# Kernel tuning notes

Hardware: AMD Instinct MI355X
Metric: run time of the kernel (lower is better)

## Reference

```python
import jax, jax.numpy as jnp
import numpy as np

B, T, DM, DH, DD, V, K = 2, 512, 1024, 4096, 4, 32000, 8
THR = 0.25
EPS = 1e-5
IGN = -100


def setup_inputs() -> dict:
    key = jax.random.key(0)
    ks = jax.random.split(key, 12)
    s = 0.02
    return {
        "H": jax.random.normal(ks[0], (B, T, DM), jnp.float32),
        "input_ids": jax.random.randint(ks[1], (B, T), 0, V),
        "attention_mask": jax.random.randint(ks[2], (B, T), 0, 2),
        "labels": jax.random.randint(ks[3], (B, T), 0, V),
        "emb": s * jax.random.normal(ks[4], (V, DM), jnp.float32),
        "depth_emb": s * jax.random.normal(ks[5], (DD, DM), jnp.float32),
        "ln_g": jnp.ones((DM,), jnp.float32),
        "ln_b": jnp.zeros((DM,), jnp.float32),
        "W1": s * jax.random.normal(ks[6], (DM, DH), jnp.float32),
        "b1": jnp.zeros((DH,), jnp.float32),
        "W2": s * jax.random.normal(ks[7], (DH, DM), jnp.float32),
        "b2": jnp.zeros((DM,), jnp.float32),
        "Wq": s * jax.random.normal(ks[8], (DM, V), jnp.float32),
        "bq": jnp.zeros((V,), jnp.float32),
        "Wb": s * jax.random.normal(ks[9], (DM, 1), jnp.float32),
        "bb": jnp.zeros((1,), jnp.float32),
    }


def _forward(H, input_ids, attention_mask, labels, emb, depth_emb, ln_g, ln_b, W1, b1, W2, b2, Wq, bq, Wb, bb):
    mask = attention_mask.astype(bool)  # (B,T)
    E = emb[input_ids]  # (B,T,DM)
    # draft state: broadcast over depth dim
    S = H[:, :, None, :] + E[:, :, None, :] + depth_emb[None, None]  # (B,T,DD,DM)
    mu = S.mean(-1, keepdims=True)
    var = ((S - mu) ** 2).mean(-1, keepdims=True)  # biased var, as torch LayerNorm
    S = (S - mu) * jax.lax.rsqrt(var + EPS) * ln_g + ln_b
    S = jax.nn.gelu(S @ W1 + b1, approximate=False) @ W2 + b2
    q = S @ Wq + bq  # (B,T,DD,V)
    beta = (S @ Wb + bb)[..., 0]  # (B,T,DD)
    q = jnp.where(mask[:, :, None, None], q, 0.0)
    beta = jnp.where(mask[:, :, None], beta, 0.0)
    # future labels for D depths (small fixed loop over DD)
    targets = jnp.full((B, T, DD), IGN, jnp.int32)
    valid = jnp.zeros((B, T, DD), bool)
    for d in range(1, DD + 1):
        v = mask[:, : T - d] & mask[:, d:]
        valid = valid.at[:, : T - d, d - 1].set(v)
        targets = targets.at[:, : T - d, d - 1].set(
            jnp.where(v, labels[:, d:].astype(jnp.int32), IGN))
    # token CE over valid positions (masked mean)
    logp = jax.nn.log_softmax(q, axis=-1)
    safe = jnp.where(valid, targets, 0)
    nll = -jnp.take_along_axis(logp, safe[..., None], axis=-1)[..., 0]
    cnt = valid.sum()
    L_q = jnp.where(cnt > 0, (nll * valid).sum() / jnp.maximum(cnt, 1).astype(q.dtype), jnp.zeros((), q.dtype))
    # BCE-with-logits on beta, averaged over valid source positions
    bce = jnp.logaddexp(0.0, beta) - beta * valid.astype(beta.dtype)
    src = valid.any(-1, keepdims=True)
    denom = jnp.maximum(src.sum(), 1).astype(beta.dtype)
    L_beta = (bce * src).sum() / denom
    return q, beta, L_q + L_beta


def reference(H, input_ids, attention_mask, labels, emb, depth_emb, ln_g, ln_b, W1, b1, W2, b2, Wq, bq, Wb, bb):
    q, beta, loss = _forward(H, input_ids, attention_mask, labels, emb, depth_emb,
                             ln_g, ln_b, W1, b1, W2, b2, Wq, bq, Wb, bb)
    # dynamic_branch_width
    sigma = jax.nn.sigmoid(beta)
    k = jnp.clip(jnp.ceil(sigma * float(K)).astype(jnp.int32), 1, K)
    k = jnp.where(sigma >= THR, k, 0)
    k = jnp.where(attention_mask.astype(bool)[:, :, None], k, 0)
    return q, beta, k, loss
```

## Files before the change

kernel.cpp:

```cpp
#include <hip/hip_runtime.h>
#include <math.h>

#define B_ 2
#define T_ 512
#define DM_ 1024
#define DH_ 4096
#define DD_ 4
#define V_ 32000
#define M_ 4096
#define BT_ 1024

typedef __attribute__((ext_vector_type(8))) unsigned short ushort8_t;
typedef __attribute__((ext_vector_type(4))) unsigned short ushort4_t;
typedef __attribute__((ext_vector_type(8))) __bf16 bf16x8;
typedef __attribute__((ext_vector_type(4))) float f32x4;

__device__ __forceinline__ unsigned short f2bf(float x) {
  union { float f; unsigned u; } v; v.f = x;
  unsigned r = v.u + 0x7fffu + ((v.u >> 16) & 1u);
  return (unsigned short)(r >> 16);
}
__device__ __forceinline__ float bf2f(unsigned short h) {
  union { unsigned u; float f; } v; v.u = ((unsigned)h) << 16; return v.f;
}

__device__ __forceinline__ float block_sum256(float v, float* sh) {
  #pragma unroll
  for (int o = 32; o >= 1; o >>= 1) v += __shfl_down(v, o);
  int lane = threadIdx.x & 63, wid = threadIdx.x >> 6;
  if (lane == 0) sh[wid] = v;
  __syncthreads();
  float t = sh[0] + sh[1] + sh[2] + sh[3];
  __syncthreads();
  return t;
}
__device__ __forceinline__ float block_max256(float v, float* sh) {
  #pragma unroll
  for (int o = 32; o >= 1; o >>= 1) v = fmaxf(v, __shfl_down(v, o));
  int lane = threadIdx.x & 63, wid = threadIdx.x >> 6;
  if (lane == 0) sh[wid] = v;
  __syncthreads();
  float t = fmaxf(fmaxf(sh[0], sh[1]), fmaxf(sh[2], sh[3]));
  __syncthreads();
  return t;
}

__global__ __launch_bounds__(256) void transpose_split_kernel(
    const float* __restrict__ in, int R, int C,
    unsigned short* __restrict__ out_hi, unsigned short* __restrict__ out_lo)
{
  __shared__ float tile[32][33];
  int c0 = blockIdx.x * 32, r0 = blockIdx.y * 32;
  int tx = threadIdx.x & 31, ty = threadIdx.x >> 5;
  #pragma unroll
  for (int i = 0; i < 4; ++i)
    tile[ty + i * 8][tx] = in[(size_t)(r0 + ty + i * 8) * C + c0 + tx];
  __syncthreads();
  #pragma unroll
  for (int i = 0; i < 4; ++i) {
    int orow = c0 + ty + i * 8;
    int ocol = r0 + tx;
    float v = tile[tx][ty + i * 8];
    unsigned short h = f2bf(v);
    out_hi[(size_t)orow * R + ocol] = h;
    if (out_lo) out_lo[(size_t)orow * R + ocol] = f2bf(v - bf2f(h));
  }
}

__global__ __launch_bounds__(256) void embed_ln_kernel(
    const float* __restrict__ H, const int* __restrict__ ids,
    const float* __restrict__ emb, const float* __restrict__ demb,
    const float* __restrict__ g, const float* __restrict__ be,
    unsigned short* __restrict__ Xhi, unsigned short* __restrict__ Xlo)
{
  __shared__ float sh[8];
  int m = blockIdx.x, tid = threadIdx.x;
  int bt = m >> 2, d = m & 3;
  int id = ids[bt];
  float4 x  = ((const float4*)(H   + (size_t)bt * DM_))[tid];
  float4 e  = ((const float4*)(emb + (size_t)id * DM_))[tid];
  float4 de = ((const float4*)(demb + (size_t)d * DM_))[tid];
  float v0 = x.x + e.x + de.x, v1 = x.y + e.y + de.y;
  float v2 = x.z + e.z + de.z, v3 = x.w + e.w + de.w;
  float mu = block_sum256((v0 + v1) + (v2 + v3), sh) * (1.0f / DM_);
  float d0 = v0 - mu, d1v = v1 - mu, d2 = v2 - mu, d3 = v3 - mu;
  float var = block_sum256((d0 * d0 + d1v * d1v) + (d2 * d2 + d3 * d3), sh) * (1.0f / DM_);
  float rs = rsqrtf(var + 1e-5f);
  float4 gg  = ((const float4*)g)[tid];
  float4 bb4 = ((const float4*)be)[tid];
  float y0 = d0 * rs * gg.x + bb4.x;
  float y1 = d1v * rs * gg.y + bb4.y;
  float y2 = d2 * rs * gg.z + bb4.z;
  float y3 = d3 * rs * gg.w + bb4.w;
  unsigned short h0 = f2bf(y0), h1 = f2bf(y1), h2 = f2bf(y2), h3 = f2bf(y3);
  ushort4_t hv = {h0, h1, h2, h3};
  ushort4_t lv = {f2bf(y0 - bf2f(h0)), f2bf(y1 - bf2f(h1)), f2bf(y2 - bf2f(h2)), f2bf(y3 - bf2f(h3))};
  size_t base = (size_t)m * DM_ + tid * 4;
  *(ushort4_t*)&Xhi[base] = hv;
  *(ushort4_t*)&Xlo[base] = lv;
}

__global__ __launch_bounds__(64) void w2b_kernel(
    const float* __restrict__ W2, const float* __restrict__ Wb,
    const float* __restrict__ b2, const float* __restrict__ bb,
    float* __restrict__ w2b)
{
  int j = blockIdx.x, lane = threadIdx.x;
  const float* rowp = (j < DH_) ? (W2 + (size_t)j * DM_) : b2;
  const float4* r4 = (const float4*)rowp;
  const float4* w4 = (const float4*)Wb;
  float s = 0.0f;
  for (int i = lane; i < DM_ / 4; i += 64) {
    float4 a = r4[i], w = w4[i];
    s += a.x * w.x + a.y * w.y + a.z * w.z + a.w * w.w;
  }
  #pragma unroll
  for (int o = 32; o >= 1; o >>= 1) s += __shfl_down(s, o);
  if (lane == 0) w2b[j] = (j < DH_) ? s : (s + bb[0]);
}

template<bool SPLIT, bool GELU>
__global__ __launch_bounds__(256) void gemm_kernel(
    const unsigned short* __restrict__ Ahi, const unsigned short* __restrict__ Alo,
    const unsigned short* __restrict__ Bhi, const unsigned short* __restrict__ Blo,
    const float* __restrict__ bias, int Ndim, int Kdim,
    float* __restrict__ Cf, unsigned short* __restrict__ Chi, unsigned short* __restrict__ Clo,
    const int* __restrict__ rowmask)
{
  constexpr int LDT = 40;
  __shared__ __align__(16) unsigned short sAhi[128 * LDT];
  __shared__ __align__(16) unsigned short sBhi[128 * LDT];
  __shared__ __align__(16) unsigned short sAlo[SPLIT ? 128 * LDT : 8];
  __shared__ __align__(16) unsigned short sBlo[SPLIT ? 128 * LDT : 8];
  const int n0 = blockIdx.x * 128, m0 = blockIdx.y * 128;
  const int tid = threadIdx.x, lane = tid & 63, wid = tid >> 6;
  const int wr = wid >> 1, wc = wid & 1;
  const int lrow = lane & 15, koff = (lane >> 4) * 8;
  const int rr = tid >> 2, cc = (tid & 3) * 8;

  f32x4 acc[4][4] = {};

  for (int k0 = 0; k0 < Kdim; k0 += 32) {
    __syncthreads();
    #pragma unroll
    for (int ch = 0; ch < 2; ++ch) {
      int r = rr + ch * 64;
      size_t ga = (size_t)(m0 + r) * Kdim + (k0 + cc);
      size_t gb = (size_t)(n0 + r) * Kdim + (k0 + cc);
      *(ushort8_t*)&sAhi[r * LDT + cc] = *(const ushort8_t*)&Ahi[ga];
      *(ushort8_t*)&sBhi[r * LDT + cc] = *(const ushort8_t*)&Bhi[gb];
      if constexpr (SPLIT) {
        *(ushort8_t*)&sAlo[r * LDT + cc] = *(const ushort8_t*)&Alo[ga];
        *(ushort8_t*)&sBlo[r * LDT + cc] = *(const ushort8_t*)&Blo[gb];
      }
    }
    __syncthreads();
    bf16x8 ah[4], bh[4], al[4], bl[4];
    #pragma unroll
    for (int i = 0; i < 4; ++i) {
      ah[i] = __builtin_bit_cast(bf16x8, *(const ushort8_t*)&sAhi[(wr * 64 + i * 16 + lrow) * LDT + koff]);
      bh[i] = __builtin_bit_cast(bf16x8, *(const ushort8_t*)&sBhi[(wc * 64 + i * 16 + lrow) * LDT + koff]);
      if constexpr (SPLIT) {
        al[i] = __builtin_bit_cast(bf16x8, *(const ushort8_t*)&sAlo[(wr * 64 + i * 16 + lrow) * LDT + koff]);
        bl[i] = __builtin_bit_cast(bf16x8, *(const ushort8_t*)&sBlo[(wc * 64 + i * 16 + lrow) * LDT + koff]);
      }
    }
    #pragma unroll
    for (int mi = 0; mi < 4; ++mi)
      #pragma unroll
      for (int ni = 0; ni < 4; ++ni) {
        acc[mi][ni] = __builtin_amdgcn_mfma_f32_16x16x32_bf16(ah[mi], bh[ni], acc[mi][ni], 0, 0, 0);
        if constexpr (SPLIT) {
          acc[mi][ni] = __builtin_amdgcn_mfma_f32_16x16x32_bf16(ah[mi], bl[ni], acc[mi][ni], 0, 0, 0);
          acc[mi][ni] = __builtin_amdgcn_mfma_f32_16x16x32_bf16(al[mi], bh[ni], acc[mi][ni], 0, 0, 0);
          acc[mi][ni] = __builtin_amdgcn_mfma_f32_16x16x32_bf16(al[mi], bl[ni], acc[mi][ni], 0, 0, 0);
        }
      }
  }

  #pragma unroll
  for (int mi = 0; mi < 4; ++mi) {
    #pragma unroll
    for (int ni = 0; ni < 4; ++ni) {
      int rbase = m0 + wr * 64 + mi * 16 + (lane >> 4) * 4;
      int col = n0 + wc * 64 + ni * 16 + (lane & 15);
      float bv = bias ? bias[col] : 0.0f;
      #pragma unroll
      for (int r2 = 0; r2 < 4; ++r2) {
        int gm = rbase + r2;
        float v = acc[mi][ni][r2] + bv;
        if constexpr (GELU) v = 0.5f * v * (1.0f + erff(v * 0.70710678118654752440f));
        if (rowmask) v *= (rowmask[gm >> 2] ? 1.0f : 0.0f);
        size_t idx = (size_t)gm * Ndim + col;
        if (Cf) Cf[idx] = v;
        if (Chi) {
          unsigned short h = f2bf(v);
          Chi[idx] = h;
          if (Clo) Clo[idx] = f2bf(v - bf2f(h));
        }
      }
    }
  }
}

__global__ __launch_bounds__(256) void beta_k_kernel(
    const float* __restrict__ act, const float* __restrict__ w2b,
    const int* __restrict__ mask,
    float* __restrict__ beta_out, float* __restrict__ k_out,
    float* __restrict__ bce, int* __restrict__ validf)
{
  __shared__ float sh[8];
  int m = blockIdx.x, tid = threadIdx.x;
  const float4* a4 = (const float4*)(act + (size_t)m * DH_);
  const float4* w4 = (const float4*)w2b;
  float s = 0.0f;
  for (int i = tid; i < DH_ / 4; i += 256) {
    float4 a = a4[i], w = w4[i];
    s += a.x * w.x + a.y * w.y + a.z * w.z + a.w * w.w;
  }
  float tot = block_sum256(s, sh);
  if (tid == 0) {
    int bt = m >> 2, d1 = (m & 3) + 1;
    float beta = tot + w2b[DH_];
    int mv = mask[bt];
    float bm = mv ? beta : 0.0f;
    int t = bt % T_;
    int valid = (t + d1 < T_) && mv && mask[bt + d1];
    beta_out[m] = bm;
    float sp = fmaxf(bm, 0.0f) + log1pf(expf(-fabsf(bm)));
    bce[m] = sp - (valid ? bm : 0.0f);
    validf[m] = valid;
    float sig = 1.0f / (1.0f + expf(-bm));
    int kk = (int)ceilf(sig * 8.0f);
    kk = kk < 1 ? 1 : (kk > 8 ? 8 : kk);
    if (!(sig >= 0.25f)) kk = 0;
    if (!mv) kk = 0;
    k_out[m] = (float)kk;
  }
}

__global__ __launch_bounds__(256) void ce_kernel(
    const float* __restrict__ q, const int* __restrict__ validf,
    const int* __restrict__ labels, float* __restrict__ nll)
{
  __shared__ float sh[8];
  int m = blockIdx.x, tid = threadIdx.x;
  if (!validf[m]) { if (tid == 0) nll[m] = 0.0f; return; }
  int bt = m >> 2, d1 = (m & 3) + 1;
  const float* row = q + (size_t)m * V_;
  float mx = -3.4e38f;
  for (int c = tid; c < V_; c += 256) mx = fmaxf(mx, row[c]);
  mx = block_max256(mx, sh);
  float s = 0.0f;
  for (int c = tid; c < V_; c += 256) s += expf(row[c] - mx);
  s = block_sum256(s, sh);
  if (tid == 0) {
    int tgt = labels[bt + d1];
    nll[m] = -(row[tgt] - mx - logf(s));
  }
}

__global__ __launch_bounds__(256) void loss_kernel(
    const float* __restrict__ nll, const int* __restrict__ validf,
    const float* __restrict__ bce, float* __restrict__ loss_out)
{
  __shared__ float sh[8];
  int tid = threadIdx.x;
  float snll = 0.0f, fcnt = 0.0f, sbce = 0.0f, fnsrc = 0.0f;
  for (int m = tid; m < M_; m += 256) { snll += nll[m]; fcnt += (float)validf[m]; }
  for (int bt = tid; bt < BT_; bt += 256) {
    int base = bt * 4;
    int src = validf[base] | validf[base + 1] | validf[base + 2] | validf[base + 3];
    if (src) { sbce += bce[base] + bce[base + 1] + bce[base + 2] + bce[base + 3]; fnsrc += 1.0f; }
  }
  snll = block_sum256(snll, sh);
  fcnt = block_sum256(fcnt, sh);
  sbce = block_sum256(sbce, sh);
  fnsrc = block_sum256(fnsrc, sh);
  if (tid == 0) {
    float Lq = fcnt > 0.0f ? snll / fcnt : 0.0f;
    float Lb = sbce / fmaxf(fnsrc, 1.0f);
    loss_out[0] = Lq + Lb;
  }
}

extern "C" void kernel_launch(void* const* d_in, const int* in_sizes, int n_in,
                              void* d_out, int out_size, void* d_ws, size_t ws_size,
                              hipStream_t stream) {
  const float* H    = (const float*)d_in[0];
  const int*   ids  = (const int*)d_in[1];
  const int*   mask = (const int*)d_in[2];
  const int*   labels = (const int*)d_in[3];
  const float* emb  = (const float*)d_in[4];
  const float* demb = (const float*)d_in[5];
  const float* ln_g = (const float*)d_in[6];
  const float* ln_b = (const float*)d_in[7];
  const float* W1   = (const float*)d_in[8];
  const float* b1   = (const float*)d_in[9];
  const float* W2   = (const float*)d_in[10];
  const float* b2   = (const float*)d_in[11];
  const float* Wq   = (const float*)d_in[12];
  const float* bq   = (const float*)d_in[13];
  const float* Wb   = (const float*)d_in[14];
  const float* bb   = (const float*)d_in[15];

  char* ws = (char*)d_ws; size_t off = 0;
  auto walloc = [&](size_t bytes) -> void* {
    void* p = ws + off; off = (off + bytes + 255) & ~(size_t)255; return p;
  };
  unsigned short* W1t_hi = (unsigned short*)walloc((size_t)DH_ * DM_ * 2);
  unsigned short* W1t_lo = (unsigned short*)walloc((size_t)DH_ * DM_ * 2);
  unsigned short* W2t_hi = (unsigned short*)walloc((size_t)DM_ * DH_ * 2);
  unsigned short* W2t_lo = (unsigned short*)walloc((size_t)DM_ * DH_ * 2);
  unsigned short* Wqt_hi = (unsigned short*)walloc((size_t)V_ * DM_ * 2);
  unsigned short* Xhi    = (unsigned short*)walloc((size_t)M_ * DM_ * 2);
  unsigned short* Xlo    = (unsigned short*)walloc((size_t)M_ * DM_ * 2);
  unsigned short* S2hi   = (unsigned short*)walloc((size_t)M_ * DM_ * 2);
  float* w2b   = (float*)walloc((DH_ + 1) * 4);
  float* nll   = (float*)walloc(M_ * 4);
  float* bcev  = (float*)walloc(M_ * 4);
  int*   validf = (int*)walloc(M_ * 4);

  float* q_out    = (float*)d_out;
  float* beta_out = q_out + (size_t)M_ * V_;
  float* k_out    = beta_out + M_;
  float* loss_out = k_out + M_;
  unsigned short* act_hi = (unsigned short*)d_out;
  unsigned short* act_lo = act_hi + (size_t)M_ * DH_;
  float*          act_f  = (float*)(act_lo + (size_t)M_ * DH_);

  transpose_split_kernel<<<dim3(DH_ / 32, DM_ / 32), 256, 0, stream>>>(W1, DM_, DH_, W1t_hi, W1t_lo);
  transpose_split_kernel<<<dim3(DM_ / 32, DH_ / 32), 256, 0, stream>>>(W2, DH_, DM_, W2t_hi, W2t_lo);
  transpose_split_kernel<<<dim3(V_ / 32, DM_ / 32), 256, 0, stream>>>(Wq, DM_, V_, Wqt_hi, nullptr);
  embed_ln_kernel<<<M_, 256, 0, stream>>>(H, ids, emb, demb, ln_g, ln_b, Xhi, Xlo);
  w2b_kernel<<<DH_ + 1, 64, 0, stream>>>(W2, Wb, b2, bb, w2b);
  gemm_kernel<true, true><<<dim3(DH_ / 128, M_ / 128), 256, 0, stream>>>(
      Xhi, Xlo, W1t_hi, W1t_lo, b1, DH_, DM_, act_f, act_hi, act_lo, nullptr);
  beta_k_kernel<<<M_, 256, 0, stream>>>(act_f, w2b, mask, beta_out, k_out, bcev, validf);
  gemm_kernel<true, false><<<dim3(DM_ / 128, M_ / 128), 256, 0, stream>>>(
      act_hi, act_lo, W2t_hi, W2t_lo, b2, DM_, DH_, nullptr, S2hi, nullptr, nullptr);
  gemm_kernel<false, false><<<dim3(V_ / 128, M_ / 128), 256, 0, stream>>>(
      S2hi, nullptr, Wqt_hi, nullptr, bq, V_, DM_, q_out, nullptr, nullptr, mask);
  ce_kernel<<<M_, 256, 0, stream>>>(q_out, validf, labels, nll);
  loss_kernel<<<1, 256, 0, stream>>>(nll, validf, bcev, loss_out);
}
```

Measured before the change: 1.668 ms.

## Fuse softmax and beta partials into GEMM epilogues, use direct LDS loads

The row-wise softmax max/sum and the beta dot product are computed as per-tile partials inside the GEMM epilogues, with small reduction kernels replacing full passes over q and the fp32 activation buffer. The fp32 activation write is removed. Tiles are staged with global_load_lds into unpadded LDS, the grid is swapped so row tiles vary fastest, q is written with nontemporal stores, and the lo*lo MFMA term of the split-precision product is dropped. This trades a full re-read of the large logits tensor and some precision for extra partial buffers. Unpadded LDS may cause bank conflicts.

```diff
diff --git a/kernel.cpp b/kernel.cpp
--- a/kernel.cpp
+++ b/kernel.cpp
@@ -9,6 +9,7 @@
 #define V_ 32000
 #define M_ 4096
 #define BT_ 1024
+#define NCHUNK_ 250
 
 typedef __attribute__((ext_vector_type(8))) unsigned short ushort8_t;
 typedef __attribute__((ext_vector_type(4))) unsigned short ushort4_t;
@@ -22,6 +23,22 @@
 }
 __device__ __forceinline__ float bf2f(unsigned short h) {
   union { unsigned u; float f; } v; v.u = ((unsigned)h) << 16; return v.f;
+}
+
+__device__ __forceinline__ void gload16(const void* g, void* l) {
+  __builtin_amdgcn_global_load_lds(
+      (const __attribute__((address_space(1))) void*)g,
+      (__attribute__((address_space(3))) void*)l, 16, 0, 0);
+}
+
+__device__ __forceinline__ void stage_tile(const unsigned short* src, int ld,
+                                           unsigned short* lds, int wid, int lane) {
+  #pragma unroll
+  for (int c = 0; c < 2; ++c) {
+    const int rbase = c * 64 + wid * 16;
+    const unsigned short* g = src + (size_t)(rbase + (lane >> 2)) * ld + (lane & 3) * 8;
+    gload16(g, lds + rbase * 32);
+  }
 }
 
 __device__ __forceinline__ float block_sum256(float v, float* sh) {
@@ -31,16 +48,6 @@
   if (lane == 0) sh[wid] = v;
   __syncthreads();
   float t = sh[0] + sh[1] + sh[2] + sh[3];
-  __syncthreads();
-  return t;
-}
-__device__ __forceinline__ float block_max256(float v, float* sh) {
-  #pragma unroll
-  for (int o = 32; o >= 1; o >>= 1) v = fmaxf(v, __shfl_down(v, o));
-  int lane = threadIdx.x & 63, wid = threadIdx.x >> 6;
-  if (lane == 0) sh[wid] = v;
-  __syncthreads();
-  float t = fmaxf(fmaxf(sh[0], sh[1]), fmaxf(sh[2], sh[3]));
   __syncthreads();
   return t;
 }
@@ -119,50 +126,53 @@
   if (lane == 0) w2b[j] = (j < DH_) ? s : (s + bb[0]);
 }
 
-template<bool SPLIT, bool GELU>
+template<bool SPLIT, bool GELU, bool CEPART, bool BETAPART, bool NTC>
 __global__ __launch_bounds__(256) void gemm_kernel(
     const unsigned short* __restrict__ Ahi, const unsigned short* __restrict__ Alo,
     const unsigned short* __restrict__ Bhi, const unsigned short* __restrict__ Blo,
     const float* __restrict__ bias, int Ndim, int Kdim,
     float* __restrict__ Cf, unsigned short* __restrict__ Chi, unsigned short* __restrict__ Clo,
-    const int* __restrict__ rowmask)
-{
-  constexpr int LDT = 40;
-  __shared__ __align__(16) unsigned short sAhi[128 * LDT];
-  __shared__ __align__(16) unsigned short sBhi[128 * LDT];
-  __shared__ __align__(16) unsigned short sAlo[SPLIT ? 128 * LDT : 8];
-  __shared__ __align__(16) unsigned short sBlo[SPLIT ? 128 * LDT : 8];
-  const int n0 = blockIdx.x * 128, m0 = blockIdx.y * 128;
+    const int* __restrict__ rowmask,
+    const float* __restrict__ w2bv, float* __restrict__ bpart,
+    float* __restrict__ pmax, float* __restrict__ psum)
+{
+  __shared__ __align__(16) unsigned short sAhi[128 * 32];
+  __shared__ __align__(16) unsigned short sBhi[128 * 32];
+  __shared__ __align__(16) unsigned short sAlo[SPLIT ? 128 * 32 : 8];
+  __shared__ __align__(16) unsigned short sBlo[SPLIT ? 128 * 32 : 8];
+  __shared__ float red[(CEPART || BETAPART) ? 512 : 8];
+
+  const int m0 = blockIdx.x * 128, n0 = blockIdx.y * 128;
   const int tid = threadIdx.x, lane = tid & 63, wid = tid >> 6;
   const int wr = wid >> 1, wc = wid & 1;
-  const int lrow = lane & 15, koff = (lane >> 4) * 8;
-  const int rr = tid >> 2, cc = (tid & 3) * 8;
+  const int lrow = lane & 15, koff = (lane >> 4) * 8, q4 = lane >> 4;
+
+  const unsigned short* Ab  = Ahi + (size_t)m0 * Kdim;
+  const unsigned short* Bb  = Bhi + (size_t)n0 * Kdim;
+  const unsigned short* Alb = SPLIT ? (Alo + (size_t)m0 * Kdim) : nullptr;
+  const unsigned short* Blb = SPLIT ? (Blo + (size_t)n0 * Kdim) : nullptr;
 
   f32x4 acc[4][4] = {};
 
   for (int k0 = 0; k0 < Kdim; k0 += 32) {
     __syncthreads();
-    #pragma unroll
-    for (int ch = 0; ch < 2; ++ch) {
-      int r = rr + ch * 64;
-      size_t ga = (size_t)(m0 + r) * Kdim + (k0 + cc);
-      size_t gb = (size_t)(n0 + r) * Kdim + (k0 + cc);
-      *(ushort8_t*)&sAhi[r * LDT + cc] = *(const ushort8_t*)&Ahi[ga];
-      *(ushort8_t*)&sBhi[r * LDT + cc] = *(const ushort8_t*)&Bhi[gb];
-      if constexpr (SPLIT) {
-        *(ushort8_t*)&sAlo[r * LDT + cc] = *(const ushort8_t*)&Alo[ga];
-        *(ushort8_t*)&sBlo[r * LDT + cc] = *(const ushort8_t*)&Blo[gb];
-      }
+    stage_tile(Ab + k0, Kdim, sAhi, wid, lane);
+    stage_tile(Bb + k0, Kdim, sBhi, wid, lane);
+    if constexpr (SPLIT) {
+      stage_tile(Alb + k0, Kdim, sAlo, wid, lane);
+      stage_tile(Blb + k0, Kdim, sBlo, wid, lane);
     }
+    asm volatile("s_waitcnt vmcnt(0)" ::: "memory");
     __syncthreads();
+
     bf16x8 ah[4], bh[4], al[4], bl[4];
     #pragma unroll
     for (int i = 0; i < 4; ++i) {
-      ah[i] = __builtin_bit_cast(bf16x8, *(const ushort8_t*)&sAhi[(wr * 64 + i * 16 + lrow) * LDT + koff]);
-      bh[i] = __builtin_bit_cast(bf16x8, *(const ushort8_t*)&sBhi[(wc * 64 + i * 16 + lrow) * LDT + koff]);
+      ah[i] = __builtin_bit_cast(bf16x8, *(const ushort8_t*)&sAhi[(wr * 64 + i * 16 + lrow) * 32 + koff]);
+      bh[i] = __builtin_bit_cast(bf16x8, *(const ushort8_t*)&sBhi[(wc * 64 + i * 16 + lrow) * 32 + koff]);
       if constexpr (SPLIT) {
-        al[i] = __builtin_bit_cast(bf16x8, *(const ushort8_t*)&sAlo[(wr * 64 + i * 16 + lrow) * LDT + koff]);
-        bl[i] = __builtin_bit_cast(bf16x8, *(const ushort8_t*)&sBlo[(wc * 64 + i * 16 + lrow) * LDT + koff]);
+        al[i] = __builtin_bit_cast(bf16x8, *(const ushort8_t*)&sAlo[(wr * 64 + i * 16 + lrow) * 32 + koff]);
+        bl[i] = __builtin_bit_cast(bf16x8, *(const ushort8_t*)&sBlo[(wc * 64 + i * 16 + lrow) * 32 + koff]);
       }
     }
     #pragma unroll
@@ -173,26 +183,28 @@
         if constexpr (SPLIT) {
           acc[mi][ni] = __builtin_amdgcn_mfma_f32_16x16x32_bf16(ah[mi], bl[ni], acc[mi][ni], 0, 0, 0);
           acc[mi][ni] = __builtin_amdgcn_mfma_f32_16x16x32_bf16(al[mi], bh[ni], acc[mi][ni], 0, 0, 0);
-          acc[mi][ni] = __builtin_amdgcn_mfma_f32_16x16x32_bf16(al[mi], bl[ni], acc[mi][ni], 0, 0, 0);
         }
       }
   }
 
   #pragma unroll
-  for (int mi = 0; mi < 4; ++mi) {
+  for (int mi = 0; mi < 4; ++mi)
     #pragma unroll
     for (int ni = 0; ni < 4; ++ni) {
-      int rbase = m0 + wr * 64 + mi * 16 + (lane >> 4) * 4;
-      int col = n0 + wc * 64 + ni * 16 + (lane & 15);
-      float bv = bias ? bias[col] : 0.0f;
+      const int col = n0 + wc * 64 + ni * 16 + lrow;
+      const float bv = bias ? bias[col] : 0.0f;
       #pragma unroll
       for (int r2 = 0; r2 < 4; ++r2) {
-        int gm = rbase + r2;
+        const int gm = m0 + wr * 64 + mi * 16 + q4 * 4 + r2;
         float v = acc[mi][ni][r2] + bv;
         if constexpr (GELU) v = 0.5f * v * (1.0f + erff(v * 0.70710678118654752440f));
         if (rowmask) v *= (rowmask[gm >> 2] ? 1.0f : 0.0f);
-        size_t idx = (size_t)gm * Ndim + col;
-        if (Cf) Cf[idx] = v;
+        acc[mi][ni][r2] = v;
+        const size_t idx = (size_t)gm * Ndim + col;
+        if (Cf) {
+          if constexpr (NTC) __builtin_nontemporal_store(v, &Cf[idx]);
+          else Cf[idx] = v;
+        }
         if (Chi) {
           unsigned short h = f2bf(v);
           Chi[idx] = h;
@@ -200,28 +212,78 @@
         }
       }
     }
-  }
-}
-
-__global__ __launch_bounds__(256) void beta_k_kernel(
-    const float* __restrict__ act, const float* __restrict__ w2b,
+
+  if constexpr (CEPART) {
+    #pragma unroll
+    for (int mi = 0; mi < 4; ++mi)
+      #pragma unroll
+      for (int r2 = 0; r2 < 4; ++r2) {
+        float mx = fmaxf(fmaxf(acc[mi][0][r2], acc[mi][1][r2]),
+                         fmaxf(acc[mi][2][r2], acc[mi][3][r2]));
+        #pragma unroll
+        for (int o = 1; o < 16; o <<= 1) mx = fmaxf(mx, __shfl_xor(mx, o));
+        float sm = 0.0f;
+        #pragma unroll
+        for (int ni = 0; ni < 4; ++ni) sm += expf(acc[mi][ni][r2] - mx);
+        #pragma unroll
+        for (int o = 1; o < 16; o <<= 1) sm += __shfl_xor(sm, o);
+        if (lrow == 0) {
+          int r64 = mi * 16 + q4 * 4 + r2;
+          red[((wr * 64 + r64) * 2 + wc) * 2 + 0] = mx;
+          red[((wr * 64 + r64) * 2 + wc) * 2 + 1] = sm;
+        }
+      }
+    __syncthreads();
+    if (tid < 128) {
+      int wr2 = tid >> 6, r64 = tid & 63;
+      float ma = red[((wr2 * 64 + r64) * 2 + 0) * 2 + 0], sa = red[((wr2 * 64 + r64) * 2 + 0) * 2 + 1];
+      float mb = red[((wr2 * 64 + r64) * 2 + 1) * 2 + 0], sb = red[((wr2 * 64 + r64) * 2 + 1) * 2 + 1];
+      float mg = fmaxf(ma, mb);
+      float sg = sa * expf(ma - mg) + sb * expf(mb - mg);
+      int grow = m0 + wr2 * 64 + r64;
+      pmax[(size_t)grow * 256 + blockIdx.y] = mg;
+      psum[(size_t)grow * 256 + blockIdx.y] = sg;
+    }
+  }
+
+  if constexpr (BETAPART) {
+    #pragma unroll
+    for (int mi = 0; mi < 4; ++mi)
+      #pragma unroll
+      for (int r2 = 0; r2 < 4; ++r2) {
+        float s = 0.0f;
+        #pragma unroll
+        for (int ni = 0; ni < 4; ++ni) {
+          const int col = n0 + wc * 64 + ni * 16 + lrow;
+          s += acc[mi][ni][r2] * w2bv[col];
+        }
+        #pragma unroll
+        for (int o = 1; o < 16; o <<= 1) s += __shfl_xor(s, o);
+        if (lrow == 0)
+          red[((wr * 64 + mi * 16 + q4 * 4 + r2) * 2 + wc) * 2 + 0] = s;
+      }
+    __syncthreads();
+    if (tid < 128) {
+      int wr2 = tid >> 6, r64 = tid & 63;
+      float s = red[((wr2 * 64 + r64) * 2 + 0) * 2 + 0] + red[((wr2 * 64 + r64) * 2 + 1) * 2 + 0];
+      bpart[(size_t)(m0 + wr2 * 64 + r64) * 32 + blockIdx.y] = s;
+    }
+  }
+}
+
+__global__ __launch_bounds__(64) void beta_k_kernel(
+    const float* __restrict__ bpart, const float* __restrict__ w2b,
     const int* __restrict__ mask,
     float* __restrict__ beta_out, float* __restrict__ k_out,
     float* __restrict__ bce, int* __restrict__ validf)
 {
-  __shared__ float sh[8];
-  int m = blockIdx.x, tid = threadIdx.x;
-  const float4* a4 = (const float4*)(act + (size_t)m * DH_);
-  const float4* w4 = (const float4*)w2b;
-  float s = 0.0f;
-  for (int i = tid; i < DH_ / 4; i += 256) {
-    float4 a = a4[i], w = w4[i];
-    s += a.x * w.x + a.y * w.y + a.z * w.z + a.w * w.w;
-  }
-  float tot = block_sum256(s, sh);
-  if (tid == 0) {
+  int m = blockIdx.x, lane = threadIdx.x;
+  float s = (lane < 32) ? bpart[(size_t)m * 32 + lane] : 0.0f;
+  #pragma unroll
+  for (int o = 32; o >= 1; o >>= 1) s += __shfl_down(s, o);
+  if (lane == 0) {
     int bt = m >> 2, d1 = (m & 3) + 1;
-    float beta = tot + w2b[DH_];
+    float beta = s + w2b[DH_];
     int mv = mask[bt];
     float bm = mv ? beta : 0.0f;
     int t = bt % T_;
@@ -239,24 +301,31 @@
   }
 }
 
-__global__ __launch_bounds__(256) void ce_kernel(
+__global__ __launch_bounds__(64) void ce_reduce_kernel(
+    const float* __restrict__ pmax, const float* __restrict__ psum,
     const float* __restrict__ q, const int* __restrict__ validf,
     const int* __restrict__ labels, float* __restrict__ nll)
 {
-  __shared__ float sh[8];
-  int m = blockIdx.x, tid = threadIdx.x;
-  if (!validf[m]) { if (tid == 0) nll[m] = 0.0f; return; }
-  int bt = m >> 2, d1 = (m & 3) + 1;
-  const float* row = q + (size_t)m * V_;
-  float mx = -3.4e38f;
-  for (int c = tid; c < V_; c += 256) mx = fmaxf(mx, row[c]);
-  mx = block_max256(mx, sh);
-  float s = 0.0f;
-  for (int c = tid; c < V_; c += 256) s += expf(row[c] - mx);
-  s = block_sum256(s, sh);
-  if (tid == 0) {
-    int tgt = labels[bt + d1];
-    nll[m] = -(row[tgt] - mx - logf(s));
+  int m = blockIdx.x, lane = threadIdx.x;
+  if (!validf[m]) { if (lane == 0) nll[m] = 0.0f; return; }
+  float ml = -3.4e38f, sl = 0.0f;
+  for (int j = lane; j < NCHUNK_; j += 64) {
+    float mj = pmax[(size_t)m * 256 + j], sj = psum[(size_t)m * 256 + j];
+    float nm = fmaxf(ml, mj);
+    sl = sl * expf(ml - nm) + sj * expf(mj - nm);
+    ml = nm;
+  }
+  #pragma unroll
+  for (int o = 32; o >= 1; o >>= 1) {
+    float mo = __shfl_xor(ml, o), so = __shfl_xor(sl, o);
+    float nm = fmaxf(ml, mo);
+    sl = sl * expf(ml - nm) + so * expf(mo - nm);
+    ml = nm;
+  }
+  if (lane == 0) {
+    int bt = m >> 2, d1 = (m & 3) + 1;
+    float qt = q[(size_t)m * V_ + labels[bt + d1]];
+    nll[m] = -(qt - ml - logf(sl));
   }
 }
 
@@ -316,9 +385,12 @@
   unsigned short* Xhi    = (unsigned short*)walloc((size_t)M_ * DM_ * 2);
   unsigned short* Xlo    = (unsigned short*)walloc((size_t)M_ * DM_ * 2);
   unsigned short* S2hi   = (unsigned short*)walloc((size_t)M_ * DM_ * 2);
-  float* w2b   = (float*)walloc((DH_ + 1) * 4);
-  float* nll   = (float*)walloc(M_ * 4);
-  float* bcev  = (float*)walloc(M_ * 4);
+  float* w2b    = (float*)walloc((DH_ + 1) * 4);
+  float* bpart  = (float*)walloc((size_t)M_ * 32 * 4);
+  float* pmax   = (float*)walloc((size_t)M_ * 256 * 4);
+  float* psum   = (float*)walloc((size_t)M_ * 256 * 4);
+  float* nll    = (float*)walloc(M_ * 4);
+  float* bcev   = (float*)walloc(M_ * 4);
   int*   validf = (int*)walloc(M_ * 4);
 
   float* q_out    = (float*)d_out;
@@ -327,20 +399,22 @@
   float* loss_out = k_out + M_;
   unsigned short* act_hi = (unsigned short*)d_out;
   unsigned short* act_lo = act_hi + (size_t)M_ * DH_;
-  float*          act_f  = (float*)(act_lo + (size_t)M_ * DH_);
 
   transpose_split_kernel<<<dim3(DH_ / 32, DM_ / 32), 256, 0, stream>>>(W1, DM_, DH_, W1t_hi, W1t_lo);
   transpose_split_kernel<<<dim3(DM_ / 32, DH_ / 32), 256, 0, stream>>>(W2, DH_, DM_, W2t_hi, W2t_lo);
   transpose_split_kernel<<<dim3(V_ / 32, DM_ / 32), 256, 0, stream>>>(Wq, DM_, V_, Wqt_hi, nullptr);
   embed_ln_kernel<<<M_, 256, 0, stream>>>(H, ids, emb, demb, ln_g, ln_b, Xhi, Xlo);
   w2b_kernel<<<DH_ + 1, 64, 0, stream>>>(W2, Wb, b2, bb, w2b);
-  gemm_kernel<true, true><<<dim3(DH_ / 128, M_ / 128), 256, 0, stream>>>(
-      Xhi, Xlo, W1t_hi, W1t_lo, b1, DH_, DM_, act_f, act_hi, act_lo, nullptr);
-  beta_k_kernel<<<M_, 256, 0, stream>>>(act_f, w2b, mask, beta_out, k_out, bcev, validf);
-  gemm_kernel<true, false><<<dim3(DM_ / 128, M_ / 128), 256, 0, stream>>>(
-      act_hi, act_lo, W2t_hi, W2t_lo, b2, DM_, DH_, nullptr, S2hi, nullptr, nullptr);
-  gemm_kernel<false, false><<<dim3(V_ / 128, M_ / 128), 256, 0, stream>>>(
-      S2hi, nullptr, Wqt_hi, nullptr, bq, V_, DM_, q_out, nullptr, nullptr, mask);
-  ce_kernel<<<M_, 256, 0, stream>>>(q_out, validf, labels, nll);
+  gemm_kernel<true, true, false, true, false><<<dim3(M_ / 128, DH_ / 128), 256, 0, stream>>>(
+      Xhi, Xlo, W1t_hi, W1t_lo, b1, DH_, DM_, nullptr, act_hi, act_lo, nullptr,
+      w2b, bpart, nullptr, nullptr);
+  beta_k_kernel<<<M_, 64, 0, stream>>>(bpart, w2b, mask, beta_out, k_out, bcev, validf);
+  gemm_kernel<true, false, false, false, false><<<dim3(M_ / 128, DM_ / 128), 256, 0, stream>>>(
+      act_hi, act_lo, W2t_hi, W2t_lo, b2, DM_, DH_, nullptr, S2hi, nullptr, nullptr,
+      nullptr, nullptr, nullptr, nullptr);
+  gemm_kernel<false, false, true, false, true><<<dim3(M_ / 128, V_ / 128), 256, 0, stream>>>(
+      S2hi, nullptr, Wqt_hi, nullptr, bq, V_, DM_, q_out, nullptr, nullptr, mask,
+      nullptr, nullptr, pmax, psum);
+  ce_reduce_kernel<<<M_, 64, 0, stream>>>(pmax, psum, q_out, validf, labels, nll);
   loss_kernel<<<1, 256, 0, stream>>>(nll, validf, bcev, loss_out);
 }
```

Measured after the change: 1.695 ms. About the same (+1.6%).
